# Optimization experiments

Measured on AMD Instinct MI355X. Metric: run time of the kernel, lower is better.

## Reference

```python
import jax, jax.numpy as jnp
import numpy as np

D_MODEL, N_LEVELS, N_HEADS, N_POINTS = 128, 3, 16, 4
D_HEAD = D_MODEL // N_HEADS


def _bilinear_sample(v, loc, H, W):
    # v: (B, H*W, nH, d) flattened level feature; loc: (B, Lq, nH, P, 2) in [0,1]
    # Matches F.grid_sample(mode='bilinear', padding_mode='zeros', align_corners=False)
    B, Lq, nH, P, _ = loc.shape
    x = loc[..., 0] * W - 0.5
    y = loc[..., 1] * H - 0.5
    x0 = jnp.floor(x)
    y0 = jnp.floor(y)
    x0i = x0.astype(jnp.int32)
    y0i = y0.astype(jnp.int32)
    out = jnp.zeros((B, Lq, P, nH, v.shape[-1]), dtype=v.dtype)
    for dx in (0, 1):
        for dy in (0, 1):
            xi = x0i + dx
            yi = y0i + dy
            wx = (x0 + 1.0 - x) if dx == 0 else (x - x0)
            wy = (y0 + 1.0 - y) if dy == 0 else (y - y0)
            valid = (xi >= 0) & (xi < W) & (yi >= 0) & (yi < H)
            w = wx * wy * valid.astype(v.dtype)           # (B,Lq,nH,P)
            idx = jnp.clip(yi, 0, H - 1) * W + jnp.clip(xi, 0, W - 1)
            idx_f = idx.transpose(0, 1, 3, 2).reshape(B, Lq * P, nH)[..., None]
            g = jnp.take_along_axis(v, idx_f, axis=1).reshape(B, Lq, P, nH, -1)
            out = out + g * w.transpose(0, 1, 3, 2)[..., None]
    return out  # (B, Lq, P, nH, d)


def _msda(fms, W_off, b_off, W_attn, b_attn, W_val, b_val, W_out, b_out):
    shapes = [(f.shape[2], f.shape[3]) for f in fms]
    B = fms[0].shape[0]
    # flatten to (B, Len, C)
    x = jnp.concatenate([f.reshape(B, D_MODEL, -1).transpose(0, 2, 1) for f in fms], axis=1)
    Lq = x.shape[1]
    # reference points (normalized pixel centers per level)
    refs = []
    for (H, W) in shapes:
        yv = (jnp.arange(H, dtype=jnp.float32) + 0.5) / H
        xv = (jnp.arange(W, dtype=jnp.float32) + 0.5) / W
        yy, xx = jnp.meshgrid(yv, xv, indexing='ij')
        refs.append(jnp.stack([xx, yy], -1).reshape(-1, 2))
    ref = jnp.concatenate(refs, 0)  # (Len, 2) in (x, y)

    value = (x @ W_val + b_val).reshape(B, Lq, N_HEADS, D_HEAD)
    offs = (x @ W_off + b_off).reshape(B, Lq, N_HEADS, N_LEVELS, N_POINTS, 2)
    attn = (x @ W_attn + b_attn).reshape(B, Lq, N_HEADS, N_LEVELS * N_POINTS)
    attn = jax.nn.softmax(attn, axis=-1).reshape(B, Lq, N_HEADS, N_LEVELS, N_POINTS)

    norm = jnp.array([[w, h] for (h, w) in shapes], dtype=jnp.float32)  # (L, 2) = (W, H)
    loc = ref[None, :, None, None, None, :] + offs / norm[None, None, None, :, None, :]

    out = jnp.zeros((B, Lq, N_HEADS, D_HEAD), dtype=x.dtype)
    start = 0
    for l, (H, W) in enumerate(shapes):
        v_l = value[:, start:start + H * W]             # (B, HW, nH, d)
        sampled = _bilinear_sample(v_l, loc[:, :, :, l], H, W)  # (B,Lq,P,nH,d)
        out = out + jnp.einsum('bqphd,bqhp->bqhd', sampled, attn[:, :, :, l, :])
        start += H * W
    out = out.reshape(B, Lq, D_MODEL) @ W_out + b_out
    return out, shapes, B


def setup_inputs() -> dict:
    key = jax.random.key(0)
    ks = jax.random.split(key, 11)
    d = {
        'feature_map1': jax.random.normal(ks[0], (8, 128, 64, 64), jnp.float32),
        'feature_map2': jax.random.normal(ks[1], (8, 128, 32, 32), jnp.float32),
        'feature_map3': jax.random.normal(ks[2], (8, 128, 16, 16), jnp.float32),
        'W_off': jax.random.normal(ks[3], (D_MODEL, N_HEADS * N_LEVELS * N_POINTS * 2), jnp.float32) * 0.01,
        'b_off': jax.random.normal(ks[4], (N_HEADS * N_LEVELS * N_POINTS * 2,), jnp.float32) * 0.5,
        'W_attn': jax.random.normal(ks[5], (D_MODEL, N_HEADS * N_LEVELS * N_POINTS), jnp.float32) * 0.02,
        'b_attn': jnp.zeros((N_HEADS * N_LEVELS * N_POINTS,), jnp.float32),
        'W_val': jax.random.normal(ks[6], (D_MODEL, D_MODEL), jnp.float32) * 0.05,
        'b_val': jnp.zeros((D_MODEL,), jnp.float32),
        'W_out': jax.random.normal(ks[7], (D_MODEL, D_MODEL), jnp.float32) * 0.05,
        'b_out': jnp.zeros((D_MODEL,), jnp.float32),
    }
    return d


def reference(feature_map1, feature_map2, feature_map3, W_off, b_off, W_attn, b_attn, W_val, b_val, W_out, b_out):
    out, shapes, B = _msda([feature_map1, feature_map2, feature_map3],
                           W_off, b_off, W_attn, b_attn, W_val, b_val, W_out, b_out)
    # split back into the 3 feature maps (B, C, H, W)
    outs = []
    start = 0
    for (H, W) in shapes:
        o = out[:, start:start + H * W].transpose(0, 2, 1).reshape(B, D_MODEL, H, W)
        outs.append(o)
        start += H * W
    return tuple(outs)
```

## Files before the change

### kernel.cpp

```cpp
#include <hip/hip_runtime.h>

#define LQ 5376
#define DM 128
#define NH 16
#define NL 3
#define NP 4
#define DH 8

typedef __attribute__((ext_vector_type(8))) short short8;
typedef __attribute__((ext_vector_type(4))) float float4_t;
typedef __attribute__((ext_vector_type(4))) unsigned int uint4_t;

__device__ __forceinline__ unsigned short f2bf(float f) {
    unsigned u = __builtin_bit_cast(unsigned, f);
    unsigned r = (u + 0x7fffu + ((u >> 16) & 1u)) >> 16;
    return (unsigned short)r;
}
__device__ __forceinline__ float bf2f(unsigned short h) {
    return __builtin_bit_cast(float, (unsigned)h << 16);
}

__device__ __forceinline__ void q_to_level(int q, int& l, int& p, int& Hl, int& Wl,
                                           int& wshift) {
    if (q < 4096)      { l = 0; p = q;        Hl = 64; Wl = 64; wshift = 6; }
    else if (q < 5120) { l = 1; p = q - 4096; Hl = 32; Wl = 32; wshift = 5; }
    else               { l = 2; p = q - 5120; Hl = 16; Wl = 16; wshift = 4; }
}

__global__ __launch_bounds__(256) void convw_k(const float* __restrict__ Wv,
                                               const float* __restrict__ Wo,
                                               const float* __restrict__ Wa,
                                               const float* __restrict__ Wout,
                                               unsigned short* __restrict__ Wvh,
                                               unsigned short* __restrict__ Woa,
                                               unsigned short* __restrict__ Wouth,
                                               unsigned short* __restrict__ Woutl) {
    int idx = blockIdx.x * 256 + threadIdx.x;
    if (idx >= 832 * 128) return;
    int col = idx >> 7;
    int k   = idx & 127;
    if (col < 128) {
        Wvh[col * 128 + k] = f2bf(Wv[k * 128 + col]);
    } else if (col < 512) {
        int c = col - 128;
        Woa[c * 128 + k] = f2bf(Wo[k * 384 + c]);
    } else if (col < 704) {
        int c = col - 512;
        Woa[(384 + c) * 128 + k] = f2bf(Wa[k * 192 + c]);
    } else {
        int c = col - 704;
        float v = Wout[k * 128 + c];
        unsigned short h = f2bf(v);
        Wouth[c * 128 + k] = h;
        Woutl[c * 128 + k] = f2bf(v - bf2f(h));
    }
}

__global__ __launch_bounds__(256) void transpose_all_k(const float* __restrict__ fm1,
                                                       const float* __restrict__ fm2,
                                                       const float* __restrict__ fm3,
                                                       unsigned short* __restrict__ xh) {
    __shared__ float tile[32][33];
    const int bx = blockIdx.x;
    const float* fm; int HW, qstart, p0;
    if (bx < 128)      { fm = fm1; HW = 4096; qstart = 0;    p0 = bx * 32; }
    else if (bx < 160) { fm = fm2; HW = 1024; qstart = 4096; p0 = (bx - 128) * 32; }
    else               { fm = fm3; HW = 256;  qstart = 5120; p0 = (bx - 160) * 32; }
    const int c0 = blockIdx.y * 32;
    const int b  = blockIdx.z;
    const int tx = threadIdx.x;
    const int ty = threadIdx.y;
    const float* src = fm + ((size_t)(b * DM + c0)) * HW + p0;
#pragma unroll
    for (int k = 0; k < 32; k += 8)
        tile[ty + k][tx] = src[(size_t)(ty + k) * HW + tx];
    __syncthreads();
    const size_t dbase = ((size_t)(b * LQ + qstart + p0)) * DM + c0;
#pragma unroll
    for (int k = 0; k < 32; k += 8)
        xh[dbase + (size_t)(ty + k) * DM + tx] = f2bf(tile[tx][ty + k]);
}

__global__ __launch_bounds__(256) void value_proj_mfma(const unsigned short* __restrict__ xh,
                                                       const unsigned short* __restrict__ Wvh,
                                                       const float* __restrict__ b_val,
                                                       unsigned short* __restrict__ valh) {
    __shared__ unsigned short vs[64][136];
    const int t = threadIdx.x;
    const int wv = t >> 6;
    const int lane = t & 63;
    const int m = lane & 15, quad = lane >> 4;
    const int q0 = blockIdx.x * 64 + wv * 16;

    short8 ah[4];
    const size_t arow = (size_t)(q0 + m) * DM;
#pragma unroll
    for (int kk = 0; kk < 4; ++kk)
        ah[kk] = *(const short8*)(xh + arow + kk * 32 + quad * 8);
    float4_t acc[8];
#pragma unroll
    for (int tt = 0; tt < 8; ++tt) acc[tt] = (float4_t)(0.f);
#pragma unroll
    for (int tt = 0; tt < 8; ++tt) {
        const size_t brow = (size_t)(tt * 16 + m) * DM;
#pragma unroll
        for (int kk = 0; kk < 4; ++kk) {
            short8 bh = *(const short8*)(Wvh + brow + kk * 32 + quad * 8);
            acc[tt] = __builtin_amdgcn_mfma_f32_16x16x32_bf16(ah[kk], bh, acc[tt], 0, 0, 0);
        }
    }
#pragma unroll
    for (int tt = 0; tt < 8; ++tt) {
        const int col = tt * 16 + m;
        const float bb = b_val[col];
#pragma unroll
        for (int r = 0; r < 4; ++r)
            vs[wv * 16 + quad * 4 + r][col] = f2bf(acc[tt][r] + bb);
    }
    __syncthreads();

    const int bq = blockIdx.x * 64;
    const int b = bq / LQ;
    const int pos0 = bq - b * LQ;
    const int h  = t >> 4;
    const int ql = t & 15;
#pragma unroll
    for (int it = 0; it < 4; ++it) {
        const int qloc = it * 16 + ql;
        uint4_t v = *(const uint4_t*)&vs[qloc][h * 8];
        *(uint4_t*)(valh + ((size_t)(h * 8 + b) * LQ + pos0 + qloc) * 8) = v;
    }
}

__global__ __launch_bounds__(256) void sampler_k(const unsigned short* __restrict__ xh,
                                                 const unsigned short* __restrict__ valh,
                                                 const unsigned short* __restrict__ Woa,
                                                 const float* __restrict__ b_off,
                                                 const float* __restrict__ b_attn,
                                                 const unsigned short* __restrict__ Wouth,
                                                 const unsigned short* __restrict__ Woutl,
                                                 const float* __restrict__ b_out,
                                                 float* __restrict__ out) {
    __shared__ float coef[16][16][37];
    __shared__ float oh[16][132];
    const int t = threadIdx.x;
    const int wv = t >> 6;
    const int lane = t & 63;
    const int m = lane & 15, quad = lane >> 4;
    const int bid = blockIdx.x;
    const int lb = (bid & 7) * 336 + (bid >> 3);
    const int gq0 = lb * 16;

    {
        short8 af[4];
        const size_t arow = (size_t)(gq0 + m) * DM;
#pragma unroll
        for (int kk = 0; kk < 4; ++kk)
            af[kk] = *(const short8*)(xh + arow + kk * 32 + quad * 8);
        float4_t acc[9];
#pragma unroll
        for (int tt = 0; tt < 9; ++tt) acc[tt] = (float4_t)(0.f);
#pragma unroll
        for (int tt = 0; tt < 9; ++tt) {
            const size_t brow = (size_t)((wv * 9 + tt) * 16 + m) * DM;
#pragma unroll
            for (int kk = 0; kk < 4; ++kk) {
                short8 bf = *(const short8*)(Woa + brow + kk * 32 + quad * 8);
                acc[tt] = __builtin_amdgcn_mfma_f32_16x16x32_bf16(af[kk], bf, acc[tt], 0, 0, 0);
            }
        }
#pragma unroll
        for (int tt = 0; tt < 9; ++tt) {
            const int col = (wv * 9 + tt) * 16 + m;
            int hc, jc;
            float bb;
            if (col < 384) { hc = col / 24; jc = col - hc * 24; bb = b_off[col]; }
            else { int cc = col - 384; hc = cc / 12; jc = 24 + cc - hc * 12; bb = b_attn[cc]; }
#pragma unroll
            for (int r = 0; r < 4; ++r)
                coef[quad * 4 + r][hc][jc] = acc[tt][r] + bb;
        }
    }
    __syncthreads();

    {
        float* a = &coef[t >> 4][t & 15][24];
        float mx = -1e30f;
#pragma unroll
        for (int k = 0; k < 12; ++k) mx = fmaxf(mx, a[k]);
        float s = 0.f;
#pragma unroll
        for (int k = 0; k < 12; ++k) {
            const float e = __expf(a[k] - mx);
            a[k] = e;
            s += e;
        }
        const float inv = 1.f / s;
#pragma unroll
        for (int k = 0; k < 12; ++k) a[k] *= inv;
    }
    __syncthreads();

    {
        const int qq = t >> 4;
        const int h  = t & 15;
        const int gq = gq0 + qq;
        const int b  = gq / LQ;
        const int q  = gq - b * LQ;
        int lq, p, Hq, Wq, wshift;
        q_to_level(q, lq, p, Hq, Wq, wshift);
        const float refx = ((p & (Wq - 1)) + 0.5f) / Wq;
        const float refy = ((p >> wshift) + 0.5f) / Hq;
        const float* cf = &coef[qq][h][0];
        const unsigned short* vbase = valh + ((size_t)(h * 8 + b) * LQ) * 8;
        float acc[8];
#pragma unroll
        for (int e = 0; e < 8; ++e) acc[e] = 0.f;
#pragma unroll
        for (int l = 0; l < NL; ++l) {
            const int Wl = 64 >> l;
            const int Hl = Wl;
            const int start_l = (l == 0) ? 0 : ((l == 1) ? 4096 : 5120);
            const float fxb = refx * Wl - 0.5f;
            const float fyb = refy * Hl - 0.5f;
#pragma unroll
            for (int pt = 0; pt < NP; ++pt) {
                const float ox = cf[(l * NP + pt) * 2 + 0];
                const float oy = cf[(l * NP + pt) * 2 + 1];
                const float a  = cf[24 + l * NP + pt];
                const float fx = fxb + ox;
                const float fy = fyb + oy;
                const float x0f = floorf(fx);
                const float y0f = floorf(fy);
                const int x0 = (int)x0f;
                const int y0 = (int)y0f;
                const float fx1 = fx - x0f, fy1 = fy - y0f;
                const float gx0 = (x0 >= 0 && x0 < Wl)          ? (1.f - fx1) : 0.f;
                const float gx1 = (x0 >= -1 && x0 < Wl - 1)     ? fx1 : 0.f;
                const float gy0 = (y0 >= 0 && y0 < Hl)          ? (1.f - fy1) : 0.f;
                const float gy1 = (y0 >= -1 && y0 < Hl - 1)     ? fy1 : 0.f;
                const int xc0 = min(max(x0, 0), Wl - 1);
                const int xc1 = min(max(x0 + 1, 0), Wl - 1);
                const int yc0 = min(max(y0, 0), Hl - 1);
                const int yc1 = min(max(y0 + 1, 0), Hl - 1);
                const int r0 = start_l + yc0 * Wl;
                const int r1 = start_l + yc1 * Wl;
                const uint4_t v00 = *(const uint4_t*)(vbase + (size_t)(r0 + xc0) * 8);
                const uint4_t v01 = *(const uint4_t*)(vbase + (size_t)(r0 + xc1) * 8);
                const uint4_t v10 = *(const uint4_t*)(vbase + (size_t)(r1 + xc0) * 8);
                const uint4_t v11 = *(const uint4_t*)(vbase + (size_t)(r1 + xc1) * 8);
                const float w00 = gx0 * gy0 * a;
                const float w01 = gx1 * gy0 * a;
                const float w10 = gx0 * gy1 * a;
                const float w11 = gx1 * gy1 * a;
#pragma unroll
                for (int dd = 0; dd < 4; ++dd) {
                    acc[dd * 2 + 0] += w00 * __builtin_bit_cast(float, v00[dd] << 16)
                                    +  w01 * __builtin_bit_cast(float, v01[dd] << 16)
                                    +  w10 * __builtin_bit_cast(float, v10[dd] << 16)
                                    +  w11 * __builtin_bit_cast(float, v11[dd] << 16);
                    acc[dd * 2 + 1] += w00 * __builtin_bit_cast(float, v00[dd] & 0xffff0000u)
                                    +  w01 * __builtin_bit_cast(float, v01[dd] & 0xffff0000u)
                                    +  w10 * __builtin_bit_cast(float, v10[dd] & 0xffff0000u)
                                    +  w11 * __builtin_bit_cast(float, v11[dd] & 0xffff0000u);
                }
            }
        }
#pragma unroll
        for (int e = 0; e < 8; ++e) oh[qq][h * 8 + e] = acc[e];
    }
    __syncthreads();

    {
        float4_t acc2[2];
        acc2[0] = (float4_t)(0.f);
        acc2[1] = (float4_t)(0.f);
#pragma unroll
        for (int kk = 0; kk < 4; ++kk) {
            const float4_t a0 = *(const float4_t*)&oh[m][kk * 32 + quad * 8];
            const float4_t a1 = *(const float4_t*)&oh[m][kk * 32 + quad * 8 + 4];
            short8 ahi, alo;
#pragma unroll
            for (int j = 0; j < 8; ++j) {
                const float f = (j < 4) ? a0[j] : a1[j - 4];
                const unsigned short h = f2bf(f);
                ahi[j] = (short)h;
                alo[j] = (short)f2bf(f - bf2f(h));
            }
#pragma unroll
            for (int tt = 0; tt < 2; ++tt) {
                const size_t brow = (size_t)((wv * 2 + tt) * 16 + m) * DM;
                short8 bh = *(const short8*)(Wouth + brow + kk * 32 + quad * 8);
                short8 bl = *(const short8*)(Woutl + brow + kk * 32 + quad * 8);
                acc2[tt] = __builtin_amdgcn_mfma_f32_16x16x32_bf16(ahi, bh, acc2[tt], 0, 0, 0);
                acc2[tt] = __builtin_amdgcn_mfma_f32_16x16x32_bf16(alo, bh, acc2[tt], 0, 0, 0);
                acc2[tt] = __builtin_amdgcn_mfma_f32_16x16x32_bf16(ahi, bl, acc2[tt], 0, 0, 0);
            }
        }
        const size_t lvl_base[3] = {0, 4194304, 5242880};
#pragma unroll
        for (int tt = 0; tt < 2; ++tt) {
            const int col = (wv * 2 + tt) * 16 + m;
            const float bb = b_out[col];
#pragma unroll
            for (int r = 0; r < 4; ++r) {
                const int qq = quad * 4 + r;
                const int gq = gq0 + qq;
                const int b = gq / LQ;
                const int q = gq - b * LQ;
                int lq, p, Hq, Wq, wshift;
                q_to_level(q, lq, p, Hq, Wq, wshift);
                const int HWq = Hq * Wq;
                out[lvl_base[lq] + ((size_t)(b * DM + col)) * HWq + p] = acc2[tt][r] + bb;
            }
        }
    }
}

extern "C" void kernel_launch(void* const* d_in, const int* in_sizes, int n_in,
                              void* d_out, int out_size, void* d_ws, size_t ws_size,
                              hipStream_t stream) {
    const float* fm1    = (const float*)d_in[0];
    const float* fm2    = (const float*)d_in[1];
    const float* fm3    = (const float*)d_in[2];
    const float* W_off  = (const float*)d_in[3];
    const float* b_off  = (const float*)d_in[4];
    const float* W_attn = (const float*)d_in[5];
    const float* b_attn = (const float*)d_in[6];
    const float* W_val  = (const float*)d_in[7];
    const float* b_val  = (const float*)d_in[8];
    const float* W_out  = (const float*)d_in[9];
    const float* b_out  = (const float*)d_in[10];
    float* out = (float*)d_out;

    const size_t NQ = (size_t)8 * LQ;
    unsigned short* xh    = (unsigned short*)d_ws;
    unsigned short* valh  = xh + NQ * DM;
    unsigned short* Wvh   = valh + NQ * DM;
    unsigned short* Woa   = Wvh + 128 * 128;
    unsigned short* Wouth = Woa + 576 * 128;
    unsigned short* Woutl = Wouth + 128 * 128;

    convw_k<<<416, 256, 0, stream>>>(W_val, W_off, W_attn, W_out,
                                     Wvh, Woa, Wouth, Woutl);

    transpose_all_k<<<dim3(168, 4, 8), dim3(32, 8), 0, stream>>>(fm1, fm2, fm3, xh);

    value_proj_mfma<<<672, 256, 0, stream>>>(xh, Wvh, b_val, valh);

    sampler_k<<<2688, 256, 0, stream>>>(xh, valh, Woa, b_off, b_attn,
                                        Wouth, Woutl, b_out, out);
}
```

Before: 288.8 us.

## Double sampler threads per block, splitting each head's sampling points across two lanes

The sampler block grows from 256 to 512 threads. Each (query, head) pair is now handled by two lanes, each sampling 6 of the 12 points, and the partial sums are combined with a lane shuffle. The softmax is recomputed per lane in registers, which removes a separate shared-memory pass and one barrier. The MFMA tiles of the offset/attention projection and the output projection are redistributed over 8 waves. The goal is more memory-level parallelism and shorter per-thread gather chains, at the cost of a larger block, duplicated softmax work and possibly lower occupancy from the 512-thread launch bound.

```diff
diff --git a/kernel.cpp b/kernel.cpp
--- a/kernel.cpp
+++ b/kernel.cpp
@@ -132,15 +132,15 @@
     }
 }
 
-__global__ __launch_bounds__(256) void sampler_k(const unsigned short* __restrict__ xh,
-                                                 const unsigned short* __restrict__ valh,
-                                                 const unsigned short* __restrict__ Woa,
-                                                 const float* __restrict__ b_off,
-                                                 const float* __restrict__ b_attn,
-                                                 const unsigned short* __restrict__ Wouth,
-                                                 const unsigned short* __restrict__ Woutl,
-                                                 const float* __restrict__ b_out,
-                                                 float* __restrict__ out) {
+__global__ __launch_bounds__(512) void sampler_k3(const unsigned short* __restrict__ xh,
+                                                  const unsigned short* __restrict__ valh,
+                                                  const unsigned short* __restrict__ Woa,
+                                                  const float* __restrict__ b_off,
+                                                  const float* __restrict__ b_attn,
+                                                  const unsigned short* __restrict__ Wouth,
+                                                  const unsigned short* __restrict__ Woutl,
+                                                  const float* __restrict__ b_out,
+                                                  float* __restrict__ out) {
     __shared__ float coef[16][16][37];
     __shared__ float oh[16][132];
     const int t = threadIdx.x;
@@ -157,53 +157,34 @@
 #pragma unroll
         for (int kk = 0; kk < 4; ++kk)
             af[kk] = *(const short8*)(xh + arow + kk * 32 + quad * 8);
-        float4_t acc[9];
-#pragma unroll
-        for (int tt = 0; tt < 9; ++tt) acc[tt] = (float4_t)(0.f);
-#pragma unroll
-        for (int tt = 0; tt < 9; ++tt) {
-            const size_t brow = (size_t)((wv * 9 + tt) * 16 + m) * DM;
-#pragma unroll
-            for (int kk = 0; kk < 4; ++kk) {
-                short8 bf = *(const short8*)(Woa + brow + kk * 32 + quad * 8);
-                acc[tt] = __builtin_amdgcn_mfma_f32_16x16x32_bf16(af[kk], bf, acc[tt], 0, 0, 0);
+#pragma unroll
+        for (int tl = 0; tl < 5; ++tl) {
+            const int tile = wv + (tl << 3);
+            if (tile < 36) {
+                const int col = tile * 16 + m;
+                const size_t brow = (size_t)col * DM;
+                float4_t acc = (float4_t)(0.f);
+#pragma unroll
+                for (int kk = 0; kk < 4; ++kk) {
+                    short8 bfr = *(const short8*)(Woa + brow + kk * 32 + quad * 8);
+                    acc = __builtin_amdgcn_mfma_f32_16x16x32_bf16(af[kk], bfr, acc, 0, 0, 0);
+                }
+                int hc, jc;
+                float bb;
+                if (col < 384) { hc = col / 24; jc = col - hc * 24; bb = b_off[col]; }
+                else { int cc = col - 384; hc = cc / 12; jc = 24 + cc - hc * 12; bb = b_attn[cc]; }
+#pragma unroll
+                for (int r = 0; r < 4; ++r)
+                    coef[quad * 4 + r][hc][jc] = acc[r] + bb;
             }
         }
-#pragma unroll
-        for (int tt = 0; tt < 9; ++tt) {
-            const int col = (wv * 9 + tt) * 16 + m;
-            int hc, jc;
-            float bb;
-            if (col < 384) { hc = col / 24; jc = col - hc * 24; bb = b_off[col]; }
-            else { int cc = col - 384; hc = cc / 12; jc = 24 + cc - hc * 12; bb = b_attn[cc]; }
-#pragma unroll
-            for (int r = 0; r < 4; ++r)
-                coef[quad * 4 + r][hc][jc] = acc[tt][r] + bb;
-        }
     }
     __syncthreads();
 
     {
-        float* a = &coef[t >> 4][t & 15][24];
-        float mx = -1e30f;
-#pragma unroll
-        for (int k = 0; k < 12; ++k) mx = fmaxf(mx, a[k]);
-        float s = 0.f;
-#pragma unroll
-        for (int k = 0; k < 12; ++k) {
-            const float e = __expf(a[k] - mx);
-            a[k] = e;
-            s += e;
-        }
-        const float inv = 1.f / s;
-#pragma unroll
-        for (int k = 0; k < 12; ++k) a[k] *= inv;
-    }
-    __syncthreads();
-
-    {
-        const int qq = t >> 4;
-        const int h  = t & 15;
+        const int hf = t & 1;
+        const int h  = (t >> 1) & 15;
+        const int qq = t >> 5;
         const int gq = gq0 + qq;
         const int b  = gq / LQ;
         const int q  = gq - b * LQ;
@@ -211,70 +192,85 @@
         q_to_level(q, lq, p, Hq, Wq, wshift);
         const float refx = ((p & (Wq - 1)) + 0.5f) / Wq;
         const float refy = ((p >> wshift) + 0.5f) / Hq;
+
         const float* cf = &coef[qq][h][0];
+        float at[12];
+#pragma unroll
+        for (int k = 0; k < 12; ++k) at[k] = cf[24 + k];
+        float off2[12];
+#pragma unroll
+        for (int k = 0; k < 12; ++k) off2[k] = cf[hf * 12 + k];
+        float mx = at[0];
+#pragma unroll
+        for (int k = 1; k < 12; ++k) mx = fmaxf(mx, at[k]);
+        float s = 0.f;
+#pragma unroll
+        for (int k = 0; k < 12; ++k) { at[k] = __expf(at[k] - mx); s += at[k]; }
+        const float inv = 1.f / s;
+
         const unsigned short* vbase = valh + ((size_t)(h * 8 + b) * LQ) * 8;
         float acc[8];
 #pragma unroll
         for (int e = 0; e < 8; ++e) acc[e] = 0.f;
-#pragma unroll
-        for (int l = 0; l < NL; ++l) {
+
+#pragma unroll
+        for (int jj = 0; jj < 6; ++jj) {
+            const int j = hf * 6 + jj;
+            const int l = j >> 2;
             const int Wl = 64 >> l;
-            const int Hl = Wl;
             const int start_l = (l == 0) ? 0 : ((l == 1) ? 4096 : 5120);
-            const float fxb = refx * Wl - 0.5f;
-            const float fyb = refy * Hl - 0.5f;
-#pragma unroll
-            for (int pt = 0; pt < NP; ++pt) {
-                const float ox = cf[(l * NP + pt) * 2 + 0];
-                const float oy = cf[(l * NP + pt) * 2 + 1];
-                const float a  = cf[24 + l * NP + pt];
-                const float fx = fxb + ox;
-                const float fy = fyb + oy;
-                const float x0f = floorf(fx);
-                const float y0f = floorf(fy);
-                const int x0 = (int)x0f;
-                const int y0 = (int)y0f;
-                const float fx1 = fx - x0f, fy1 = fy - y0f;
-                const float gx0 = (x0 >= 0 && x0 < Wl)          ? (1.f - fx1) : 0.f;
-                const float gx1 = (x0 >= -1 && x0 < Wl - 1)     ? fx1 : 0.f;
-                const float gy0 = (y0 >= 0 && y0 < Hl)          ? (1.f - fy1) : 0.f;
-                const float gy1 = (y0 >= -1 && y0 < Hl - 1)     ? fy1 : 0.f;
-                const int xc0 = min(max(x0, 0), Wl - 1);
-                const int xc1 = min(max(x0 + 1, 0), Wl - 1);
-                const int yc0 = min(max(y0, 0), Hl - 1);
-                const int yc1 = min(max(y0 + 1, 0), Hl - 1);
-                const int r0 = start_l + yc0 * Wl;
-                const int r1 = start_l + yc1 * Wl;
-                const uint4_t v00 = *(const uint4_t*)(vbase + (size_t)(r0 + xc0) * 8);
-                const uint4_t v01 = *(const uint4_t*)(vbase + (size_t)(r0 + xc1) * 8);
-                const uint4_t v10 = *(const uint4_t*)(vbase + (size_t)(r1 + xc0) * 8);
-                const uint4_t v11 = *(const uint4_t*)(vbase + (size_t)(r1 + xc1) * 8);
-                const float w00 = gx0 * gy0 * a;
-                const float w01 = gx1 * gy0 * a;
-                const float w10 = gx0 * gy1 * a;
-                const float w11 = gx1 * gy1 * a;
-#pragma unroll
-                for (int dd = 0; dd < 4; ++dd) {
-                    acc[dd * 2 + 0] += w00 * __builtin_bit_cast(float, v00[dd] << 16)
-                                    +  w01 * __builtin_bit_cast(float, v01[dd] << 16)
-                                    +  w10 * __builtin_bit_cast(float, v10[dd] << 16)
-                                    +  w11 * __builtin_bit_cast(float, v11[dd] << 16);
-                    acc[dd * 2 + 1] += w00 * __builtin_bit_cast(float, v00[dd] & 0xffff0000u)
-                                    +  w01 * __builtin_bit_cast(float, v01[dd] & 0xffff0000u)
-                                    +  w10 * __builtin_bit_cast(float, v10[dd] & 0xffff0000u)
-                                    +  w11 * __builtin_bit_cast(float, v11[dd] & 0xffff0000u);
-                }
+            const float aw = (hf ? at[jj + 6] : at[jj]) * inv;
+            const float ox = off2[jj * 2 + 0];
+            const float oy = off2[jj * 2 + 1];
+            const float fx = refx * Wl - 0.5f + ox;
+            const float fy = refy * Wl - 0.5f + oy;
+            const float x0f = floorf(fx);
+            const float y0f = floorf(fy);
+            const int x0 = (int)x0f;
+            const int y0 = (int)y0f;
+            const float fx1 = fx - x0f, fy1 = fy - y0f;
+            const float gx0 = (x0 >= 0 && x0 < Wl)      ? (1.f - fx1) : 0.f;
+            const float gx1 = (x0 >= -1 && x0 < Wl - 1) ? fx1 : 0.f;
+            const float gy0 = (y0 >= 0 && y0 < Wl)      ? (1.f - fy1) : 0.f;
+            const float gy1 = (y0 >= -1 && y0 < Wl - 1) ? fy1 : 0.f;
+            const int xc0 = min(max(x0, 0), Wl - 1);
+            const int xc1 = min(max(x0 + 1, 0), Wl - 1);
+            const int yc0 = min(max(y0, 0), Wl - 1);
+            const int yc1 = min(max(y0 + 1, 0), Wl - 1);
+            const int r0 = start_l + yc0 * Wl;
+            const int r1 = start_l + yc1 * Wl;
+            const uint4_t v00 = *(const uint4_t*)(vbase + (size_t)(r0 + xc0) * 8);
+            const uint4_t v01 = *(const uint4_t*)(vbase + (size_t)(r0 + xc1) * 8);
+            const uint4_t v10 = *(const uint4_t*)(vbase + (size_t)(r1 + xc0) * 8);
+            const uint4_t v11 = *(const uint4_t*)(vbase + (size_t)(r1 + xc1) * 8);
+            const float w00 = gx0 * gy0 * aw;
+            const float w01 = gx1 * gy0 * aw;
+            const float w10 = gx0 * gy1 * aw;
+            const float w11 = gx1 * gy1 * aw;
+#pragma unroll
+            for (int dd = 0; dd < 4; ++dd) {
+                acc[dd * 2 + 0] += w00 * __builtin_bit_cast(float, v00[dd] << 16)
+                                +  w01 * __builtin_bit_cast(float, v01[dd] << 16)
+                                +  w10 * __builtin_bit_cast(float, v10[dd] << 16)
+                                +  w11 * __builtin_bit_cast(float, v11[dd] << 16);
+                acc[dd * 2 + 1] += w00 * __builtin_bit_cast(float, v00[dd] & 0xffff0000u)
+                                +  w01 * __builtin_bit_cast(float, v01[dd] & 0xffff0000u)
+                                +  w10 * __builtin_bit_cast(float, v10[dd] & 0xffff0000u)
+                                +  w11 * __builtin_bit_cast(float, v11[dd] & 0xffff0000u);
             }
         }
 #pragma unroll
-        for (int e = 0; e < 8; ++e) oh[qq][h * 8 + e] = acc[e];
+        for (int e = 0; e < 8; ++e) acc[e] += __shfl_xor(acc[e], 1, 64);
+        const int ob = h * 8 + hf * 4;
+        oh[qq][ob + 0] = hf ? acc[4] : acc[0];
+        oh[qq][ob + 1] = hf ? acc[5] : acc[1];
+        oh[qq][ob + 2] = hf ? acc[6] : acc[2];
+        oh[qq][ob + 3] = hf ? acc[7] : acc[3];
     }
     __syncthreads();
 
     {
-        float4_t acc2[2];
-        acc2[0] = (float4_t)(0.f);
-        acc2[1] = (float4_t)(0.f);
+        float4_t acc2 = (float4_t)(0.f);
 #pragma unroll
         for (int kk = 0; kk < 4; ++kk) {
             const float4_t a0 = *(const float4_t*)&oh[m][kk * 32 + quad * 8];
@@ -283,36 +279,30 @@
 #pragma unroll
             for (int j = 0; j < 8; ++j) {
                 const float f = (j < 4) ? a0[j] : a1[j - 4];
-                const unsigned short h = f2bf(f);
-                ahi[j] = (short)h;
-                alo[j] = (short)f2bf(f - bf2f(h));
+                const unsigned short hh = f2bf(f);
+                ahi[j] = (short)hh;
+                alo[j] = (short)f2bf(f - bf2f(hh));
             }
-#pragma unroll
-            for (int tt = 0; tt < 2; ++tt) {
-                const size_t brow = (size_t)((wv * 2 + tt) * 16 + m) * DM;
-                short8 bh = *(const short8*)(Wouth + brow + kk * 32 + quad * 8);
-                short8 bl = *(const short8*)(Woutl + brow + kk * 32 + quad * 8);
-                acc2[tt] = __builtin_amdgcn_mfma_f32_16x16x32_bf16(ahi, bh, acc2[tt], 0, 0, 0);
-                acc2[tt] = __builtin_amdgcn_mfma_f32_16x16x32_bf16(alo, bh, acc2[tt], 0, 0, 0);
-                acc2[tt] = __builtin_amdgcn_mfma_f32_16x16x32_bf16(ahi, bl, acc2[tt], 0, 0, 0);
-            }
+            const size_t brow = (size_t)(wv * 16 + m) * DM + kk * 32 + quad * 8;
+            short8 bh = *(const short8*)(Wouth + brow);
+            short8 bl = *(const short8*)(Woutl + brow);
+            acc2 = __builtin_amdgcn_mfma_f32_16x16x32_bf16(ahi, bh, acc2, 0, 0, 0);
+            acc2 = __builtin_amdgcn_mfma_f32_16x16x32_bf16(alo, bh, acc2, 0, 0, 0);
+            acc2 = __builtin_amdgcn_mfma_f32_16x16x32_bf16(ahi, bl, acc2, 0, 0, 0);
         }
         const size_t lvl_base[3] = {0, 4194304, 5242880};
-#pragma unroll
-        for (int tt = 0; tt < 2; ++tt) {
-            const int col = (wv * 2 + tt) * 16 + m;
-            const float bb = b_out[col];
-#pragma unroll
-            for (int r = 0; r < 4; ++r) {
-                const int qq = quad * 4 + r;
-                const int gq = gq0 + qq;
-                const int b = gq / LQ;
-                const int q = gq - b * LQ;
-                int lq, p, Hq, Wq, wshift;
-                q_to_level(q, lq, p, Hq, Wq, wshift);
-                const int HWq = Hq * Wq;
-                out[lvl_base[lq] + ((size_t)(b * DM + col)) * HWq + p] = acc2[tt][r] + bb;
-            }
+        const int col = wv * 16 + m;
+        const float bb = b_out[col];
+#pragma unroll
+        for (int r = 0; r < 4; ++r) {
+            const int qq = quad * 4 + r;
+            const int gq = gq0 + qq;
+            const int b = gq / LQ;
+            const int q = gq - b * LQ;
+            int lq, p, Hq, Wq, wshift;
+            q_to_level(q, lq, p, Hq, Wq, wshift);
+            const int HWq = Hq * Wq;
+            out[lvl_base[lq] + ((size_t)(b * DM + col)) * HWq + p] = acc2[r] + bb;
         }
     }
 }
@@ -348,6 +338,6 @@
 
     value_proj_mfma<<<672, 256, 0, stream>>>(xh, Wvh, b_val, valh);
 
-    sampler_k<<<2688, 256, 0, stream>>>(xh, valh, Woa, b_off, b_attn,
-                                        Wouth, Woutl, b_out, out);
-}
+    sampler_k3<<<2688, 512, 0, stream>>>(xh, valh, Woa, b_off, b_attn,
+                                         Wouth, Woutl, b_out, out);
+}
```

New measurement: 250.0 us. 1.16x faster.
